# Performance work log

Hardware: AMD Instinct MI355X
Metric: run time of the kernel (lower is better)

Reference implementation:

```python
import jax, jax.numpy as jnp
import numpy as np

B, L, E = 64, 256, 512
H = 1024          # hidden_size
N = 128           # memory_size
HS = 64           # head_size (memory width)
NH = 4            # NTM heads
OUT = 1024        # output_size
TNH = 4           # transformer nhead
IN_DIM = E + NH * HS          # 768
POD = H + NH * HS             # 1280


def ln(x, g, b, eps=1e-5):
    mu = x.mean(-1, keepdims=True)
    v = ((x - mu) ** 2).mean(-1, keepdims=True)
    return (x - mu) / jnp.sqrt(v + eps) * g + b


def setup_inputs() -> dict:
    key = jax.random.key(0)
    ks = iter(jax.random.split(key, 64))
    def w(shape, s=0.05):
        return jax.random.normal(next(ks), shape, jnp.float32) * s
    f32 = jnp.float32
    return dict(
        x_emb=jax.random.normal(next(ks), (B, L, E), f32),
        in_g=jnp.ones(IN_DIM, f32), in_b=jnp.zeros(IN_DIM, f32),
        W_ih=w((4 * H, IN_DIM)), W_hh=w((4 * H, H)),
        b_ih=jnp.zeros(4 * H, f32), b_hh=jnp.zeros(4 * H, f32),
        cn_g=jnp.ones(H, f32), cn_b=jnp.zeros(H, f32),
        W_rk=w((NH * HS, H)), b_rk=jnp.zeros(NH * HS, f32),
        W_wk=w((NH * HS, H)), b_wk=jnp.zeros(NH * HS, f32),
        W_ws=w((NH, H)), b_ws=jnp.zeros(NH, f32),
        W_ev=w((NH * HS, H)), b_ev=jnp.zeros(NH * HS, f32),
        attn_w=w((3 * HS, HS)), attn_b=jnp.zeros(3 * HS, f32),
        attn_ow=w((HS, HS)), attn_ob=jnp.zeros(HS, f32),
        l1_w=w((2 * HS, HS)), l1_b=jnp.zeros(2 * HS, f32),
        l2_w=w((HS, 2 * HS)), l2_b=jnp.zeros(HS, f32),
        tn1_g=jnp.ones(HS, f32), tn1_b=jnp.zeros(HS, f32),
        tn2_g=jnp.ones(HS, f32), tn2_b=jnp.zeros(HS, f32),
        rkn_g=jnp.ones(HS, f32), rkn_b=jnp.zeros(HS, f32),
        wkn_g=jnp.ones(HS, f32), wkn_b=jnp.zeros(HS, f32),
        mn_g=jnp.ones(HS, f32), mn_b=jnp.zeros(HS, f32),
        po_g=jnp.ones(POD, f32), po_b=jnp.zeros(POD, f32),
        W_proj=w((OUT, POD)), b_proj=jnp.zeros(OUT, f32),
    )


def reference(x_emb, in_g, in_b, W_ih, W_hh, b_ih, b_hh, cn_g, cn_b,
              W_rk, b_rk, W_wk, b_wk, W_ws, b_ws, W_ev, b_ev,
              attn_w, attn_b, attn_ow, attn_ob, l1_w, l1_b, l2_w, l2_b,
              tn1_g, tn1_b, tn2_g, tn2_b, rkn_g, rkn_b, wkn_g, wkn_b,
              mn_g, mn_b, po_g, po_b, W_proj, b_proj):
    Bc = x_emb.shape[0]
    dh = HS // TNH

    def tblock(mem):  # [B, N, HS], eval-mode (dropout = identity)
        qkv = mem @ attn_w.T + attn_b
        q, k, v = jnp.split(qkv, 3, axis=-1)
        q = q.reshape(Bc, N, TNH, dh)
        k = k.reshape(Bc, N, TNH, dh)
        v = v.reshape(Bc, N, TNH, dh)
        a = jax.nn.softmax(jnp.einsum('bqhd,bkhd->bhqk', q, k) / jnp.sqrt(jnp.float32(dh)), axis=-1)
        o = jnp.einsum('bhqk,bkhd->bqhd', a, v).reshape(Bc, N, HS)
        o = o @ attn_ow.T + attn_ob
        x = ln(mem + o, tn1_g, tn1_b)
        ff = jax.nn.gelu(x @ l1_w.T + l1_b, approximate=False) @ l2_w.T + l2_b
        return ln(x + ff, tn2_g, tn2_b)

    def step(carry, x_t):
        h, c, mem, rc = carry
        inp = ln(jnp.concatenate([x_t, rc.reshape(Bc, -1)], axis=-1), in_g, in_b)
        gates = inp @ W_ih.T + b_ih + h @ W_hh.T + b_hh  # torch gate order i,f,g,o
        i, f, g, o = jnp.split(gates, 4, axis=-1)
        c = jax.nn.sigmoid(f) * c + jax.nn.sigmoid(i) * jnp.tanh(g)
        h = jax.nn.sigmoid(o) * jnp.tanh(c)
        hn = ln(h, cn_g, cn_b)
        rk = (hn @ W_rk.T + b_rk).reshape(Bc, NH, HS)
        wk = (hn @ W_wk.T + b_wk).reshape(Bc, NH, HS)
        ws = jax.nn.sigmoid(hn @ W_ws.T + b_ws)                    # [B, NH]
        ev = jax.nn.sigmoid(hn @ W_ev.T + b_ev).reshape(Bc, NH, HS)
        # addressing
        mem = tblock(mem)
        mem_n = ln(mem, mn_g, mn_b)
        rk = ln(rk, rkn_g, rkn_b)
        wk = ln(wk, wkn_g, wkn_b)
        rw = jax.nn.softmax(jnp.einsum('bnk,bmk->bnm', rk, mem_n), axis=-1)
        rc = jnp.einsum('bnm,bmh->bnh', rw, mem)
        ww = jax.nn.softmax(jnp.einsum('bnk,bmk->bnm', wk, mem_n), axis=-1)
        erase = jnp.einsum('bnm,bnh->bmh', ww, ev)
        mem = mem * (1.0 - erase)
        add = jnp.einsum('bnm,bnh->bmh', ww, ws[..., None] * wk)
        mem = mem + add
        out = ln(jnp.concatenate([hn, rc.reshape(Bc, -1)], axis=-1), po_g, po_b)
        logits = out @ W_proj.T + b_proj
        return (h, c, mem, rc), logits

    h0 = jnp.zeros((Bc, H), x_emb.dtype)
    c0 = jnp.zeros((Bc, H), x_emb.dtype)
    mem0 = jnp.zeros((Bc, N, HS), x_emb.dtype)
    rc0 = jnp.zeros((Bc, NH, HS), x_emb.dtype)
    (h, c, mem, _), outs = jax.lax.scan(step, (h0, c0, mem0, rc0), jnp.swapaxes(x_emb, 0, 1))
    return jnp.swapaxes(outs, 0, 1), mem, (h[None], c[None])
```

## Files before the change

kernel.cpp:

```cpp
#include <hip/hip_runtime.h>
#include <math.h>

typedef short s8v __attribute__((ext_vector_type(8)));
typedef float f32x4 __attribute__((ext_vector_type(4)));

__device__ inline float sigm(float x) { return 1.0f / (1.0f + expf(-x)); }
__device__ inline float dot4(const float4 a, const float4 b) {
  return a.x*b.x + a.y*b.y + a.z*b.z + a.w*b.w;
}
__device__ inline float wsum(float v) {
#pragma unroll
  for (int o = 32; o > 0; o >>= 1) v += __shfl_xor(v, o, 64);
  return v;
}
__device__ inline short f2bf(float f) {
  unsigned int u = __float_as_uint(f);
  unsigned int r = u + 0x7FFFu + ((u >> 16) & 1u);
  return (short)(r >> 16);
}
__device__ inline float bf2f(short h) {
  return __uint_as_float(((unsigned int)(unsigned short)h) << 16);
}
__device__ inline void storesplit(float v, short* __restrict__ hi,
                                  short* __restrict__ lo, size_t idx) {
  short h = f2bf(v);
  hi[idx] = h;
  lo[idx] = f2bf(v - bf2f(h));
}

template<int LD, int KS>
__device__ __forceinline__ void gemm4(const short* __restrict__ A,
                                      const short* __restrict__ B,
                                      f32x4 acc[4], int lane) {
  int off = (lane & 15) * LD + ((lane >> 4) * 8);
#pragma unroll 4
  for (int kb = 0; kb < KS; kb++) {
    int ko = off + kb*32;
    s8v bb = *(const s8v*)(B + ko);
#pragma unroll
    for (int m = 0; m < 4; m++) {
      s8v aa = *(const s8v*)(A + ko + m*16*LD);
      acc[m] = __builtin_amdgcn_mfma_f32_16x16x32_bf16(aa, bb, acc[m], 0,0,0);
    }
  }
}

__global__ void kprep_g(const float* __restrict__ Wih, const float* __restrict__ Whh,
                        short* __restrict__ WgH, short* __restrict__ WgL) {
  int r = blockIdx.y, k = blockIdx.x*256 + threadIdx.x;
  if (k < 1792) {
    int jt = r >> 6, rr = r & 63, ul = rr >> 2, gi = rr & 3;
    int orow = gi*1024 + jt*16 + ul;
    float v = (k < 768) ? Wih[(size_t)orow*768 + k] : Whh[(size_t)orow*1024 + (k-768)];
    storesplit(v, WgH, WgL, (size_t)r*1792 + k);
  }
}
__global__ void kprep_p(const float* __restrict__ Wp, short* __restrict__ W) {
  int j = blockIdx.y, k = blockIdx.x*256 + threadIdx.x;
  W[(size_t)j*1280 + k] = f2bf(Wp[(size_t)j*1280 + k]);
}
__global__ void kprep_h(const float* __restrict__ Wrk, const float* __restrict__ Wwk,
                        const float* __restrict__ Wev, const float* __restrict__ Wws,
                        short* __restrict__ WhH, short* __restrict__ WhL) {
  int j = blockIdx.y, k = blockIdx.x*256 + threadIdx.x;
  float v;
  if (j < 256)      v = Wrk[(size_t)j*1024 + k];
  else if (j < 512) v = Wwk[(size_t)(j-256)*1024 + k];
  else if (j < 768) v = Wev[(size_t)(j-512)*1024 + k];
  else if (j < 772) v = Wws[(size_t)(j-768)*1024 + k];
  else v = 0.f;
  storesplit(v, WhH, WhL, (size_t)j*1024 + k);
}
__global__ void kprep_q(const float* __restrict__ aw, short* __restrict__ WH,
                        short* __restrict__ WL) {
  int i = blockIdx.x*64 + threadIdx.x;
  storesplit(aw[i], WH, WL, i);
}

__global__ __launch_bounds__(256) void k_prep0(
    const float* __restrict__ x_emb, const float* __restrict__ in_g,
    const float* __restrict__ in_b, short* __restrict__ inbH,
    short* __restrict__ inbL)
{
  __shared__ float rs[4], rq[4];
  int b = blockIdx.x, tid = threadIdx.x, lane = tid & 63, wid = tid >> 6;
  float v3[3]; float s = 0.f, sq = 0.f;
#pragma unroll
  for (int i = 0; i < 3; i++) {
    int k = tid + i * 256;
    float v = (k < 512) ? x_emb[(size_t)b * 256 * 512 + k] : 0.f;
    v3[i] = v; s += v; sq += v * v;
  }
  s = wsum(s); sq = wsum(sq);
  if (lane == 0) { rs[wid] = s; rq[wid] = sq; }
  __syncthreads();
  float ts = rs[0]+rs[1]+rs[2]+rs[3], tq = rq[0]+rq[1]+rq[2]+rq[3];
  float mu = ts / 768.f, var = tq / 768.f - mu * mu;
  float rstd = rsqrtf(var + 1e-5f);
#pragma unroll
  for (int i = 0; i < 3; i++) {
    int k = tid + i * 256;
    storesplit((v3[i] - mu) * rstd * in_g[k] + in_b[k], inbH, inbL, b*1792 + k);
  }
}

__global__ __launch_bounds__(256) void kA(
    const short* __restrict__ inbH, const short* __restrict__ inbL,
    short* __restrict__ inbHn, short* __restrict__ inbLn,
    const short* __restrict__ WgH, const short* __restrict__ WgL,
    const float* __restrict__ b_ih, const float* __restrict__ b_hh,
    float* __restrict__ cbuf, float* __restrict__ hbuf,
    float* __restrict__ hstat, float* __restrict__ gatesP,
    unsigned* __restrict__ tick,
    const short* __restrict__ membH, const short* __restrict__ membL,
    const short* __restrict__ WqH, const short* __restrict__ WqL,
    const float* __restrict__ attn_b,
    const short* __restrict__ pob16, const short* __restrict__ Wp16,
    const float* __restrict__ b_proj,
    float* __restrict__ qkv, float* __restrict__ outs, int t)
{
  __shared__ char poolA[40960];
  __shared__ unsigned sOld;
  int bid = blockIdx.x, tid = threadIdx.x, lane = tid & 63, w = tid >> 6;
  if (bid < 128) {
    if (t >= 256) return;
    short (*sT)[4][2560] = (short(*)[4][2560])poolA;
    int jt = bid & 63, kt = bid >> 6;
    int k0 = kt * 896;
    int srow = tid >> 2, scol = (tid & 3) * 8;
    const short* gAH = inbH + srow*1792 + k0 + scol;
    const short* gAL = inbL + srow*1792 + k0 + scol;
    const short* gBH = WgH + (size_t)(jt*64 + srow)*1792 + k0 + scol;
    const short* gBL = WgL + (size_t)(jt*64 + srow)*1792 + k0 + scol;
    int4 rAH = *(const int4*)gAH, rAL = *(const int4*)gAL;
    int4 rBH = *(const int4*)gBH, rBL = *(const int4*)gBL;
    *(int4*)&sT[0][0][srow*40 + scol] = rAH;
    *(int4*)&sT[0][1][srow*40 + scol] = rAL;
    *(int4*)&sT[0][2][srow*40 + scol] = rBH;
    *(int4*)&sT[0][3][srow*40 + scol] = rBL;
    f32x4 acc[4] = {};
    int arow = lane & 15, akk = (lane >> 4) * 8;
    for (int c = 0; c < 28; ++c) {
      int cur = c & 1;
      if (c < 27) {
        rAH = *(const int4*)(gAH + (c+1)*32);
        rAL = *(const int4*)(gAL + (c+1)*32);
        rBH = *(const int4*)(gBH + (c+1)*32);
        rBL = *(const int4*)(gBL + (c+1)*32);
      }
      __syncthreads();
      s8v bh = *(const s8v*)&sT[cur][2][(w*16 + arow)*40 + akk];
      s8v bl = *(const s8v*)&sT[cur][3][(w*16 + arow)*40 + akk];
#pragma unroll
      for (int ms = 0; ms < 4; ++ms) {
        s8v ah = *(const s8v*)&sT[cur][0][(arow + ms*16)*40 + akk];
        s8v al = *(const s8v*)&sT[cur][1][(arow + ms*16)*40 + akk];
        acc[ms] = __builtin_amdgcn_mfma_f32_16x16x32_bf16(ah, bh, acc[ms], 0,0,0);
        acc[ms] = __builtin_amdgcn_mfma_f32_16x16x32_bf16(al, bh, acc[ms], 0,0,0);
        acc[ms] = __builtin_amdgcn_mfma_f32_16x16x32_bf16(ah, bl, acc[ms], 0,0,0);
      }
      if (c < 27) {
        *(int4*)&sT[cur^1][0][srow*40 + scol] = rAH;
        *(int4*)&sT[cur^1][1][srow*40 + scol] = rAL;
        *(int4*)&sT[cur^1][2][srow*40 + scol] = rBH;
        *(int4*)&sT[cur^1][3][srow*40 + scol] = rBL;
      }
    }
    {
      float* gp = gatesP + (size_t)kt * 262144;
      int j = jt*64 + w*16 + (lane & 15);
#pragma unroll
      for (int ms = 0; ms < 4; ms++)
#pragma unroll
        for (int r = 0; r < 4; r++) {
          int b = ms*16 + (lane>>4)*4 + r;
          gp[b*4096 + j] = acc[ms][r];
        }
    }
    __syncthreads();
    if (tid == 0) {
      __threadfence();
      sOld = __hip_atomic_fetch_add(&tick[jt], 1u, __ATOMIC_ACQ_REL,
                                    __HIP_MEMORY_SCOPE_AGENT);
    }
    __syncthreads();
    if (!(sOld & 1u)) return;
    {
      const float* pp = gatesP + (size_t)(kt^1) * 262144;
      int j = jt*64 + w*16 + (lane & 15);
#pragma unroll
      for (int ms = 0; ms < 4; ms++)
#pragma unroll
        for (int r = 0; r < 4; r++) {
          int b = ms*16 + (lane>>4)*4 + r;
          acc[ms][r] += __hip_atomic_load(&pp[b*4096 + j], __ATOMIC_RELAXED,
                                          __HIP_MEMORY_SCOPE_AGENT);
        }
    }
    float* sC = (float*)poolA;
    float* sRed = (float*)(poolA + 17408);
    __syncthreads();
    {
      int rr = w*16 + (lane & 15);
#pragma unroll
      for (int ms = 0; ms < 4; ms++)
#pragma unroll
        for (int r = 0; r < 4; r++) {
          int b = ms*16 + (lane>>4)*4 + r;
          sC[b*68 + rr] = acc[ms][r];
        }
    }
    __syncthreads();
    {
      int b = tid & 63;
      float sh = 0.f, sh2 = 0.f;
#pragma unroll
      for (int q = 0; q < 4; q++) {
        int ul = (tid >> 6) + q*4;
        int u = jt*16 + ul;
        float gi_ = sC[b*68 + ul*4 + 0] + b_ih[u]        + b_hh[u];
        float gf  = sC[b*68 + ul*4 + 1] + b_ih[1024 + u] + b_hh[1024 + u];
        float gg  = sC[b*68 + ul*4 + 2] + b_ih[2048 + u] + b_hh[2048 + u];
        float go  = sC[b*68 + ul*4 + 3] + b_ih[3072 + u] + b_hh[3072 + u];
        float cn = sigm(gf)*cbuf[b*1024 + u] + sigm(gi_)*tanhf(gg);
        float hh = sigm(go)*tanhf(cn);
        cbuf[b*1024 + u] = cn;
        hbuf[b*1024 + u] = hh;
        storesplit(hh, inbHn, inbLn, b*1792 + 768 + u);
        sh += hh; sh2 += hh*hh;
      }
      sRed[(tid>>6)*64 + b] = sh;
      sRed[256 + (tid>>6)*64 + b] = sh2;
    }
    __syncthreads();
    if (tid < 64) {
      float s0 = sRed[tid]+sRed[64+tid]+sRed[128+tid]+sRed[192+tid];
      float s1 = sRed[256+tid]+sRed[320+tid]+sRed[384+tid]+sRed[448+tid];
      hstat[(tid*64 + jt)*2]     = s0;
      hstat[(tid*64 + jt)*2 + 1] = s1;
    }
  } else if (bid < 192) {
    if (t >= 256) return;
    int b = bid - 128;
    const short* Ah = membH + (size_t)b * 8192;
    const short* Al = membL + (size_t)b * 8192;
    int ao = (w*32 + (lane & 15)) * 64 + (lane >> 4) * 8;
    s8v ah00 = *(const s8v*)(Ah + ao);
    s8v ah01 = *(const s8v*)(Ah + ao + 32);
    s8v ah10 = *(const s8v*)(Ah + ao + 16*64);
    s8v ah11 = *(const s8v*)(Ah + ao + 16*64 + 32);
    s8v al00 = *(const s8v*)(Al + ao);
    s8v al01 = *(const s8v*)(Al + ao + 32);
    s8v al10 = *(const s8v*)(Al + ao + 16*64);
    s8v al11 = *(const s8v*)(Al + ao + 16*64 + 32);
    int bo = (lane & 15) * 64 + (lane >> 4) * 8;
    for (int n = 0; n < 12; n++) {
      s8v bh0 = *(const s8v*)(WqH + bo + n*1024);
      s8v bh1 = *(const s8v*)(WqH + bo + n*1024 + 32);
      s8v bl0 = *(const s8v*)(WqL + bo + n*1024);
      s8v bl1 = *(const s8v*)(WqL + bo + n*1024 + 32);
      f32x4 acc0 = {}, acc1 = {};
      acc0 = __builtin_amdgcn_mfma_f32_16x16x32_bf16(ah00, bh0, acc0, 0,0,0);
      acc0 = __builtin_amdgcn_mfma_f32_16x16x32_bf16(ah01, bh1, acc0, 0,0,0);
      acc0 = __builtin_amdgcn_mfma_f32_16x16x32_bf16(al00, bh0, acc0, 0,0,0);
      acc0 = __builtin_amdgcn_mfma_f32_16x16x32_bf16(al01, bh1, acc0, 0,0,0);
      acc0 = __builtin_amdgcn_mfma_f32_16x16x32_bf16(ah00, bl0, acc0, 0,0,0);
      acc0 = __builtin_amdgcn_mfma_f32_16x16x32_bf16(ah01, bl1, acc0, 0,0,0);
      acc1 = __builtin_amdgcn_mfma_f32_16x16x32_bf16(ah10, bh0, acc1, 0,0,0);
      acc1 = __builtin_amdgcn_mfma_f32_16x16x32_bf16(ah11, bh1, acc1, 0,0,0);
      acc1 = __builtin_amdgcn_mfma_f32_16x16x32_bf16(al10, bh0, acc1, 0,0,0);
      acc1 = __builtin_amdgcn_mfma_f32_16x16x32_bf16(al11, bh1, acc1, 0,0,0);
      acc1 = __builtin_amdgcn_mfma_f32_16x16x32_bf16(ah10, bl0, acc1, 0,0,0);
      acc1 = __builtin_amdgcn_mfma_f32_16x16x32_bf16(ah11, bl1, acc1, 0,0,0);
      int j = n*16 + (lane & 15);
      int ch = j >> 6, jj = j & 63;
      float bv = attn_b[j];
#pragma unroll
      for (int r = 0; r < 4; r++) {
        int m0 = w*32 + (lane>>4)*4 + r;
        qkv[((size_t)(b*3 + ch)*128 + m0)*64 + jj] = acc0[r] + bv;
        qkv[((size_t)(b*3 + ch)*128 + m0 + 16)*64 + jj] = acc1[r] + bv;
      }
    }
  } else {
    if (t == 0) return;
    int jt = bid - 192;
    f32x4 acc[4] = {};
    const short* B = Wp16 + (size_t)(jt*64 + w*16) * 1280;
    gemm4<1280, 40>(pob16, B, acc, lane);
    int j = jt*64 + w*16 + (lane & 15);
    float bv = b_proj[j];
#pragma unroll
    for (int ms = 0; ms < 4; ms++)
#pragma unroll
      for (int r = 0; r < 4; r++) {
        int b = ms*16 + (lane>>4)*4 + r;
        outs[((size_t)b*256 + (t-1))*1024 + j] = acc[ms][r] + bv;
      }
  }
}

__global__ __launch_bounds__(512) void kB(
    float* __restrict__ mem, const float* __restrict__ qkv,
    const float* __restrict__ attn_ow, const float* __restrict__ attn_ob,
    const float* __restrict__ l1w, const float* __restrict__ l1b,
    const float* __restrict__ l2w, const float* __restrict__ l2b,
    const float* __restrict__ tn1g, const float* __restrict__ tn1b,
    const float* __restrict__ tn2g, const float* __restrict__ tn2b,
    const float* __restrict__ hbuf, const float* __restrict__ hstat,
    const float* __restrict__ cn_g, const float* __restrict__ cn_b,
    const short* __restrict__ WhH, const short* __restrict__ WhL,
    float* __restrict__ hp)
{
  __shared__ float pool[35200];
  int bid = blockIdx.x, tid = threadIdx.x;
  int lane = tid & 63, wid = tid >> 6;
  if (bid < 52) {
    int kt = bid & 3, jt = bid >> 2;
    {
      int b2 = tid & 63, part = tid >> 6;
      float s0 = 0.f, s1 = 0.f;
#pragma unroll 4
      for (int m2 = 0; m2 < 8; m2++) {
        int jt2 = part*8 + m2;
        s0 += hstat[(b2*64 + jt2)*2];
        s1 += hstat[(b2*64 + jt2)*2 + 1];
      }
      pool[part*64 + b2] = s0;
      pool[512 + part*64 + b2] = s1;
    }
    __syncthreads();
    if (tid < 64) {
      float ts = 0.f, tq = 0.f;
#pragma unroll
      for (int p2 = 0; p2 < 8; p2++) {
        ts += pool[p2*64 + tid];
        tq += pool[512 + p2*64 + tid];
      }
      float mu = ts / 1024.f;
      pool[1024+tid] = mu;
      pool[1088+tid] = rsqrtf(tq/1024.f - mu*mu + 1e-5f);
    }
    __syncthreads();
    short* sAH = (short*)&pool[1152];
    short* sAL = sAH + 2560;
    int srow = tid >> 3, scol = (tid & 7) * 4;
    int arow = lane & 15, akk = (lane >> 4) * 8;
    f32x4 acc[4] = {};
    for (int c = 0; c < 8; ++c) {
      __syncthreads();
      {
        float mu = pool[1024 + srow], rsd = pool[1088 + srow];
        int kbase = kt*256 + c*32 + scol;
        const float* hpt = hbuf + srow*1024 + kbase;
#pragma unroll
        for (int i = 0; i < 4; i++) {
          float hnv = (hpt[i] - mu) * rsd * cn_g[kbase + i] + cn_b[kbase + i];
          short hh = f2bf(hnv);
          sAH[srow*40 + scol + i] = hh;
          sAL[srow*40 + scol + i] = f2bf(hnv - bf2f(hh));
        }
      }
      __syncthreads();
      if (wid < 4) {
        size_t bo = (size_t)(jt*64 + wid*16 + arow)*1024 + kt*256 + c*32 + akk;
        s8v bh = *(const s8v*)(WhH + bo);
        s8v bl = *(const s8v*)(WhL + bo);
#pragma unroll
        for (int ms = 0; ms < 4; ++ms) {
          s8v ah = *(const s8v*)&sAH[(arow + ms*16)*40 + akk];
          s8v al = *(const s8v*)&sAL[(arow + ms*16)*40 + akk];
          acc[ms] = __builtin_amdgcn_mfma_f32_16x16x32_bf16(ah, bh, acc[ms], 0,0,0);
          acc[ms] = __builtin_amdgcn_mfma_f32_16x16x32_bf16(al, bh, acc[ms], 0,0,0);
          acc[ms] = __builtin_amdgcn_mfma_f32_16x16x32_bf16(ah, bl, acc[ms], 0,0,0);
        }
      }
    }
    if (wid < 4) {
      int j = jt*64 + wid*16 + (lane & 15);
#pragma unroll
      for (int ms = 0; ms < 4; ms++)
#pragma unroll
        for (int r = 0; r < 4; r++) {
          int b2 = ms*16 + (lane>>4)*4 + r;
          hp[(size_t)kt*53248 + b2*832 + j] = acc[ms][r];
        }
    }
    return;
  }
  float* sK  = pool;
  float* sV  = pool + 8704;
  float* sX  = pool + 17408;
  float* sM  = pool + 19584;
  float* sO  = pool + 21760;
  float* sS  = pool + 23936;
  float* sRed= pool + 34176;
  int bb0 = bid - 52;
  int b = bb0 & 63, mt = bb0 >> 6;
  int m0 = mt * 32;
  const float* qb = qkv + (size_t)b*3*8192;
  for (int i = tid*4; i < 8192; i += 2048) {
    *(float4*)&sK[i] = *(const float4*)&qb[8192 + i];
    *(float4*)&sV[i] = *(const float4*)&qb[16384 + i];
  }
  {
    int i = tid*4;
    int m = i >> 6, s = i & 63;
    *(float4*)&sX[m*68+s] = *(const float4*)&qb[m0*64 + i];
    *(float4*)&sM[m*68+s] = *(const float4*)&mem[(size_t)b*8192 + m0*64 + i];
  }
  __syncthreads();
  int m = tid >> 4, hd = (tid >> 2) & 3, q = tid & 3;
  const float* qp = sX + m*68 + hd*16;
  float4 q0 = *(const float4*)(qp),   q1 = *(const float4*)(qp+4);
  float4 q2 = *(const float4*)(qp+8), q3 = *(const float4*)(qp+12);
  int kmb = q * 32;
  float mx = -1e30f;
#pragma unroll 4
  for (int kk = 0; kk < 32; kk++) {
    const float* kp = sK + (kmb+kk)*64 + hd*16;
    float sc = dot4(q0, *(const float4*)kp)     + dot4(q1, *(const float4*)(kp+4))
             + dot4(q2, *(const float4*)(kp+8)) + dot4(q3, *(const float4*)(kp+12));
    mx = fmaxf(mx, sc * 0.25f);
  }
  float4 o0 = {0,0,0,0}, o1 = {0,0,0,0}, o2 = {0,0,0,0}, o3 = {0,0,0,0};
  float sum = 0.f;
#pragma unroll 4
  for (int kk = 0; kk < 32; kk++) {
    const float* kp = sK + (kmb+kk)*64 + hd*16;
    float sc = dot4(q0, *(const float4*)kp)     + dot4(q1, *(const float4*)(kp+4))
             + dot4(q2, *(const float4*)(kp+8)) + dot4(q3, *(const float4*)(kp+12));
    float e = expf(sc * 0.25f - mx);
    sum += e;
    const float* vp = sV + (kmb+kk)*64 + hd*16;
    float4 v0 = *(const float4*)vp,     v1 = *(const float4*)(vp+4);
    float4 v2 = *(const float4*)(vp+8), v3 = *(const float4*)(vp+12);
    o0.x += e*v0.x; o0.y += e*v0.y; o0.z += e*v0.z; o0.w += e*v0.w;
    o1.x += e*v1.x; o1.y += e*v1.y; o1.z += e*v1.z; o1.w += e*v1.w;
    o2.x += e*v2.x; o2.y += e*v2.y; o2.z += e*v2.z; o2.w += e*v2.w;
    o3.x += e*v3.x; o3.y += e*v3.y; o3.z += e*v3.z; o3.w += e*v3.w;
  }
  {
    float* pp = sS + tid*20;
    *(float4*)&pp[0]  = o0; *(float4*)&pp[4]  = o1;
    *(float4*)&pp[8]  = o2; *(float4*)&pp[12] = o3;
    sRed[tid] = mx; sRed[512+tid] = sum;
  }
  __syncthreads();
  if (q == 0) {
    float m1 = sRed[tid+1], m2 = sRed[tid+2], m3 = sRed[tid+3];
    float M = fmaxf(fmaxf(mx, m1), fmaxf(m2, m3));
    float e0 = expf(mx - M), e1 = expf(m1 - M), e2 = expf(m2 - M), e3 = expf(m3 - M);
    float inv = 1.0f / (sum*e0 + sRed[512+tid+1]*e1 + sRed[512+tid+2]*e2
                        + sRed[512+tid+3]*e3);
    const float* p1 = sS + (tid+1)*20;
    const float* p2 = sS + (tid+2)*20;
    const float* p3 = sS + (tid+3)*20;
    float oo[16];
    *(float4*)&oo[0] = o0; *(float4*)&oo[4] = o1;
    *(float4*)&oo[8] = o2; *(float4*)&oo[12] = o3;
    float* op = sO + m*68 + hd*16;
#pragma unroll
    for (int d = 0; d < 16; d++)
      op[d] = (oo[d]*e0 + p1[d]*e1 + p2[d]*e2 + p3[d]*e3) * inv;
  }
  __syncthreads();
  for (int idx = tid; idx < 4096; idx += 512) {
    int j = idx >> 6, s = idx & 63;
    sS[j*68 + s] = attn_ow[idx];
  }
  __syncthreads();
  {
    int mm = tid >> 4, jset = tid & 15;
    float4 orow[16];
#pragma unroll
    for (int r = 0; r < 16; r++) orow[r] = *(const float4*)&sO[mm*68 + r*4];
#pragma unroll
    for (int i = 0; i < 4; i++) {
      int j = jset + 16*i;
      const float* wr = sS + j*68;
      float acc = attn_ob[j];
#pragma unroll
      for (int r = 0; r < 16; r++) acc += dot4(orow[r], *(const float4*)&wr[r*4]);
      sM[mm*68 + j] += acc;
    }
  }
  __syncthreads();
  for (int r = wid; r < 32; r += 8) {
    float v = sM[r*68 + lane];
    float ssum = wsum(v), ssq = wsum(v*v);
    float mu = ssum*(1.f/64), var = ssq*(1.f/64) - mu*mu;
    sX[r*68+lane] = (v - mu)*rsqrtf(var+1e-5f)*tn1g[lane] + tn1b[lane];
  }
  for (int idx = tid; idx < 8192; idx += 512) {
    int f = idx >> 6, s = idx & 63;
    sK[f*68 + s] = l1w[idx];
  }
  for (int idx = tid; idx < 8192; idx += 512) {
    int j = idx >> 7, s = idx & 127;
    sV[j*132 + s] = l2w[idx];
  }
  __syncthreads();
  {
    int mm = tid >> 4, fs = tid & 15;
    float4 xr[16];
#pragma unroll
    for (int r = 0; r < 16; r++) xr[r] = *(const float4*)&sX[mm*68 + r*4];
#pragma unroll 4
    for (int i = 0; i < 8; i++) {
      int f = fs + 16*i;
      const float* wr = sK + f*68;
      float acc = l1b[f];
#pragma unroll
      for (int r = 0; r < 16; r++) acc += dot4(xr[r], *(const float4*)&wr[r*4]);
      sS[mm*132 + f] = 0.5f*acc*(1.0f + erff(acc*0.70710678118654752f));
    }
  }
  __syncthreads();
  {
    int mm = tid >> 4, jset = tid & 15;
    float acc6[4];
#pragma unroll
    for (int i = 0; i < 4; i++) acc6[i] = sX[mm*68 + jset + 16*i] + l2b[jset + 16*i];
#pragma unroll
    for (int h = 0; h < 2; h++) {
      float4 fr[16];
#pragma unroll
      for (int r = 0; r < 16; r++) fr[r] = *(const float4*)&sS[mm*132 + h*64 + r*4];
#pragma unroll
      for (int i = 0; i < 4; i++) {
        int j = jset + 16*i;
        const float* wr = sV + j*132 + h*64;
        float a = 0.f;
#pragma unroll
        for (int r = 0; r < 16; r++) a += dot4(fr[r], *(const float4*)&wr[r*4]);
        acc6[i] += a;
      }
    }
#pragma unroll
    for (int i = 0; i < 4; i++) sO[mm*68 + jset + 16*i] = acc6[i];
  }
  __syncthreads();
  for (int r = wid; r < 32; r += 8) {
    float v = sO[r*68 + lane];
    float ssum = wsum(v), ssq = wsum(v*v);
    float mu = ssum*(1.f/64), var = ssq*(1.f/64) - mu*mu;
    mem[(size_t)b*8192 + (m0+r)*64 + lane] =
        (v - mu)*rsqrtf(var+1e-5f)*tn2g[lane] + tn2b[lane];
  }
}

__global__ __launch_bounds__(512) void kC(
    float* __restrict__ mem, short* __restrict__ membH, short* __restrict__ membL,
    const float* __restrict__ hp, const float* __restrict__ hstat,
    const float* __restrict__ hbuf,
    const float* __restrict__ b_rk, const float* __restrict__ b_wk,
    const float* __restrict__ b_ev, const float* __restrict__ b_ws,
    const float* __restrict__ rkn_g, const float* __restrict__ rkn_b,
    const float* __restrict__ wkn_g, const float* __restrict__ wkn_b,
    const float* __restrict__ cn_g, const float* __restrict__ cn_b,
    const float* __restrict__ mng, const float* __restrict__ mnb,
    const float* __restrict__ pog, const float* __restrict__ pob,
    const float* __restrict__ x_emb, const float* __restrict__ in_g,
    const float* __restrict__ in_b,
    short* __restrict__ inbHn, short* __restrict__ inbLn,
    short* __restrict__ pob16, int tnext)
{
  __shared__ float P[20960];
  float* sMT  = P;
  float* sMN  = P + 8192;
  float* sHn  = P + 16512;
  float* sRk  = P + 17536;
  float* sWk  = P + 17792;
  float* sEv  = P + 18048;
  float* sWs  = P + 18304;
  float* sRw  = P + 18308;
  float* sWw  = P + 18820;
  float* sRc  = P + 19332;
  float* sRcP = P + 19588;
  float* rs   = P + 20100;
  float* rq   = P + 20108;
  float* sHst = P + 20116;
  int b = blockIdx.x, tid = threadIdx.x, lane = tid & 63, wv = tid >> 6;
  for (int i = tid*4; i < 8192; i += 2048)
    *(float4*)&sMT[i] = *(const float4*)&mem[(size_t)b*8192 + i];
  if (wv == 0) {
    float v0 = hstat[(b*64 + lane)*2], v1 = hstat[(b*64 + lane)*2 + 1];
    float s0 = wsum(v0), s1 = wsum(v1);
    if (lane == 0) {
      float mu = s0 / 1024.f;
      sHst[0] = mu;
      sHst[1] = rsqrtf(s1/1024.f - mu*mu + 1e-5f);
    }
  }
  __syncthreads();
  {
    float mu = sHst[0], rstd = sHst[1];
    for (int u = tid; u < 1024; u += 512)
      sHn[u] = (hbuf[b*1024 + u] - mu)*rstd*cn_g[u] + cn_b[u];
  }
  {
    const float* h0 = hp + (size_t)b*832;
    const float* h1 = hp + 53248 + (size_t)b*832;
    const float* h2 = hp + 2*53248 + (size_t)b*832;
    const float* h3 = hp + 3*53248 + (size_t)b*832;
    if (wv < 4) {
      int idx = wv*64 + lane;
      float v = h0[idx] + h1[idx] + h2[idx] + h3[idx] + b_rk[idx];
      float ssum = wsum(v), ssq = wsum(v*v);
      float mu = ssum*(1.f/64), var = ssq*(1.f/64) - mu*mu;
      sRk[idx] = (v - mu)*rsqrtf(var+1e-5f)*rkn_g[lane] + rkn_b[lane];
    } else {
      int idx = (wv-4)*64 + lane;
      float v = h0[256+idx] + h1[256+idx] + h2[256+idx] + h3[256+idx] + b_wk[idx];
      float ssum = wsum(v), ssq = wsum(v*v);
      float mu = ssum*(1.f/64), var = ssq*(1.f/64) - mu*mu;
      sWk[idx] = (v - mu)*rsqrtf(var+1e-5f)*wkn_g[lane] + wkn_b[lane];
    }
    if (tid < 256)
      sEv[tid] = sigm(h0[512+tid] + h1[512+tid] + h2[512+tid] + h3[512+tid] + b_ev[tid]);
    if (tid >= 256 && tid < 260) {
      int n = tid - 256;
      sWs[n] = sigm(h0[768+n] + h1[768+n] + h2[768+n] + h3[768+n] + b_ws[n]);
    }
  }
  for (int r = wv; r < 128; r += 8) {
    float v = sMT[r*64 + lane];
    float ssum = wsum(v), ssq = wsum(v*v);
    float mu = ssum*(1.f/64), var = ssq*(1.f/64) - mu*mu;
    sMN[r*65 + lane] = (v - mu)*rsqrtf(var+1e-5f)*mng[lane] + mnb[lane];
  }
  __syncthreads();
#pragma unroll
  for (int q = 0; q < 2; q++) {
    int idx = tid + q*512;
    int which = idx >> 9;
    int n = (idx >> 7) & 3, m = idx & 127;
    const float* key = (which ? sWk : sRk) + n*64;
    const float* mr = sMN + m*65;
    float acc = 0.f;
#pragma unroll 8
    for (int k = 0; k < 64; k++) acc += key[k]*mr[k];
    (which ? sWw : sRw)[n*128 + m] = acc;
  }
  __syncthreads();
  {
    float* row = (wv < 4) ? (sRw + wv*128) : (sWw + (wv-4)*128);
    float a0 = row[lane], a1 = row[lane+64];
    float mx = fmaxf(a0, a1);
#pragma unroll
    for (int o = 32; o > 0; o >>= 1) mx = fmaxf(mx, __shfl_xor(mx, o, 64));
    float e0 = expf(a0 - mx), e1 = expf(a1 - mx);
    float inv = 1.0f / wsum(e0 + e1);
    row[lane] = e0*inv; row[lane+64] = e1*inv;
  }
  __syncthreads();
  {
    int idx = tid & 255, h2 = tid >> 8;
    int n = idx >> 6, s2 = idx & 63;
    float acc = 0.f;
    for (int mm = h2*64; mm < h2*64 + 64; mm++) acc += sRw[n*128 + mm] * sMT[mm*64 + s2];
    sRcP[tid] = acc;
  }
  __syncthreads();
  if (tid < 256) sRc[tid] = sRcP[tid] + sRcP[256 + tid];
  for (int idx = tid; idx < 8192; idx += 512) {
    int mm = idx >> 6, s2 = idx & 63;
    float er = 0.f, ad = 0.f;
#pragma unroll
    for (int n = 0; n < 4; n++) {
      float w = sWw[n*128 + mm];
      er += w * sEv[n*64 + s2];
      ad += w * sWs[n] * sWk[n*64 + s2];
    }
    float val = sMT[idx]*(1.0f - er) + ad;
    mem[(size_t)b*8192 + idx] = val;
    storesplit(val, membH, membL, (size_t)b*8192 + idx);
  }
  __syncthreads();
  {
    float v5[3]; float s = 0.f, sq = 0.f;
#pragma unroll
    for (int i = 0; i < 3; i++) {
      int k = tid + i*512;
      float v = 0.f;
      if (k < 1280) v = (k < 1024) ? sHn[k] : sRc[k-1024];
      v5[i] = v; s += v; sq += v*v;
    }
    s = wsum(s); sq = wsum(sq);
    if (lane == 0) { rs[wv] = s; rq[wv] = sq; }
    __syncthreads();
    float ts = 0.f, tq = 0.f;
#pragma unroll
    for (int p = 0; p < 8; p++) { ts += rs[p]; tq += rq[p]; }
    float mu = ts/1280.f, var = tq/1280.f - mu*mu;
    float rstd = rsqrtf(var + 1e-5f);
#pragma unroll
    for (int i = 0; i < 3; i++) {
      int k = tid + i*512;
      if (k < 1280) pob16[b*1280 + k] = f2bf((v5[i] - mu)*rstd*pog[k] + pob[k]);
    }
  }
  if (tnext < 256) {
    __syncthreads();
    float v3[2]; float s2 = 0.f, q2 = 0.f;
#pragma unroll
    for (int i = 0; i < 2; i++) {
      int k = tid + i*512;
      float v = 0.f;
      if (k < 768) v = (k < 512) ? x_emb[((size_t)b*256 + tnext)*512 + k] : sRc[k-512];
      v3[i] = v; s2 += v; q2 += v*v;
    }
    s2 = wsum(s2); q2 = wsum(q2);
    if (lane == 0) { rs[wv] = s2; rq[wv] = q2; }
    __syncthreads();
    float ts = 0.f, tq = 0.f;
#pragma unroll
    for (int p = 0; p < 8; p++) { ts += rs[p]; tq += rq[p]; }
    float mu = ts/768.f, var = tq/768.f - mu*mu;
    float rstd = rsqrtf(var + 1e-5f);
#pragma unroll
    for (int i = 0; i < 2; i++) {
      int k = tid + i*512;
      if (k < 768)
        storesplit((v3[i] - mu)*rstd*in_g[k] + in_b[k], inbHn, inbLn, b*1792 + k);
    }
  }
}

__global__ void k_final(const float* __restrict__ mem, const float* __restrict__ hbuf,
                        const float* __restrict__ cbuf, float* __restrict__ out)
{
  int i = blockIdx.x * 256 + threadIdx.x;
  if (i < 524288) out[16777216 + i] = mem[i];
  if (i < 65536) {
    out[17301504 + i] = hbuf[i];
    out[17367040 + i] = cbuf[i];
  }
}

extern "C" void kernel_launch(void* const* d_in, const int* in_sizes, int n_in,
                              void* d_out, int out_size, void* d_ws, size_t ws_size,
                              hipStream_t stream) {
  const float* x_emb  = (const float*)d_in[0];
  const float* in_g   = (const float*)d_in[1];
  const float* in_b   = (const float*)d_in[2];
  const float* W_ih   = (const float*)d_in[3];
  const float* W_hh   = (const float*)d_in[4];
  const float* b_ih   = (const float*)d_in[5];
  const float* b_hh   = (const float*)d_in[6];
  const float* cn_g   = (const float*)d_in[7];
  const float* cn_b   = (const float*)d_in[8];
  const float* W_rk   = (const float*)d_in[9];
  const float* b_rk   = (const float*)d_in[10];
  const float* W_wk   = (const float*)d_in[11];
  const float* b_wk   = (const float*)d_in[12];
  const float* W_ws   = (const float*)d_in[13];
  const float* b_ws   = (const float*)d_in[14];
  const float* W_ev   = (const float*)d_in[15];
  const float* b_ev   = (const float*)d_in[16];
  const float* attn_w = (const float*)d_in[17];
  const float* attn_b = (const float*)d_in[18];
  const float* attn_ow= (const float*)d_in[19];
  const float* attn_ob= (const float*)d_in[20];
  const float* l1_w   = (const float*)d_in[21];
  const float* l1_b   = (const float*)d_in[22];
  const float* l2_w   = (const float*)d_in[23];
  const float* l2_b   = (const float*)d_in[24];
  const float* tn1_g  = (const float*)d_in[25];
  const float* tn1_b  = (const float*)d_in[26];
  const float* tn2_g  = (const float*)d_in[27];
  const float* tn2_b  = (const float*)d_in[28];
  const float* rkn_g  = (const float*)d_in[29];
  const float* rkn_b  = (const float*)d_in[30];
  const float* wkn_g  = (const float*)d_in[31];
  const float* wkn_b  = (const float*)d_in[32];
  const float* mn_g   = (const float*)d_in[33];
  const float* mn_b   = (const float*)d_in[34];
  const float* po_g   = (const float*)d_in[35];
  const float* po_b   = (const float*)d_in[36];
  const float* W_proj = (const float*)d_in[37];
  const float* b_proj = (const float*)d_in[38];

  float* ws = (float*)d_ws;
  float* mem    = ws;
  float* cbuf   = ws + 524288;
  float* hbuf   = ws + 589824;
  float* gatesP = ws + 655360;
  float* hp     = ws + 1179648;
  float* hstat  = ws + 1392640;
  unsigned* tick = (unsigned*)(ws + 1400832);
  float* qkvb   = ws + 1400896;
  short* sb     = (short*)(ws + 2973760);
  short* inbH0 = sb;
  short* inbL0 = sb + 114688;
  short* inbH1 = sb + 229376;
  short* inbL1 = sb + 344064;
  short* membH = sb + 458752;
  short* membL = sb + 983040;
  short* pob16 = sb + 1507328;
  short* WgH   = sb + 1589248;
  short* WgL   = sb + 8929280;
  short* WhH   = sb + 16269312;
  short* WhL   = sb + 17121280;
  short* WqH   = sb + 17973248;
  short* WqL   = sb + 17985536;
  short* Wp16  = sb + 17997824;

  hipMemsetAsync(ws, 0, 655360 * sizeof(float), stream);
  hipMemsetAsync(tick, 0, 256, stream);
  hipMemsetAsync(sb, 0, 1507328 * sizeof(short), stream);

  kprep_g<<<dim3(7, 4096), 256, 0, stream>>>(W_ih, W_hh, WgH, WgL);
  kprep_p<<<dim3(5, 1024), 256, 0, stream>>>(W_proj, Wp16);
  kprep_h<<<dim3(4, 832), 256, 0, stream>>>(W_rk, W_wk, W_ev, W_ws, WhH, WhL);
  kprep_q<<<dim3(192), 64, 0, stream>>>(attn_w, WqH, WqL);
  k_prep0<<<64, 256, 0, stream>>>(x_emb, in_g, in_b, inbH0, inbL0);

  float* outs = (float*)d_out;
  short* bufsH[2] = {inbH0, inbH1};
  short* bufsL[2] = {inbL0, inbL1};
  for (int t = 0; t < 256; t++) {
    kA<<<208, 256, 0, stream>>>(bufsH[t&1], bufsL[t&1], bufsH[(t+1)&1], bufsL[(t+1)&1],
                                WgH, WgL, b_ih, b_hh, cbuf, hbuf, hstat, gatesP, tick,
                                membH, membL, WqH, WqL, attn_b,
                                pob16, Wp16, b_proj, qkvb, outs, t);
    kB<<<308, 512, 0, stream>>>(mem, qkvb, attn_ow, attn_ob,
                                l1_w, l1_b, l2_w, l2_b,
                                tn1_g, tn1_b, tn2_g, tn2_b,
                                hbuf, hstat, cn_g, cn_b, WhH, WhL, hp);
    kC<<<64, 512, 0, stream>>>(mem, membH, membL, hp, hstat, hbuf,
                               b_rk, b_wk, b_ev, b_ws,
                               rkn_g, rkn_b, wkn_g, wkn_b, cn_g, cn_b,
                               mn_g, mn_b, po_g, po_b,
                               x_emb, in_g, in_b,
                               bufsH[(t+1)&1], bufsL[(t+1)&1], pob16, t+1);
  }
  kA<<<208, 256, 0, stream>>>(bufsH[0], bufsL[0], bufsH[1], bufsL[1],
                              WgH, WgL, b_ih, b_hh, cbuf, hbuf, hstat, gatesP, tick,
                              membH, membL, WqH, WqL, attn_b,
                              pob16, Wp16, b_proj, qkvb, outs, 256);
  k_final<<<2048, 256, 0, stream>>>(mem, hbuf, cbuf, (float*)d_out);
}
```

Before: 25.81 ms.

## Move head-projection GEMM into kA behind a device-wide atomic counter wait

The 52 blocks that compute the head projections (hp) from the layer-normed LSTM hidden state move from kB into kA as extra blocks. They spin on a global counter that the 64 LSTM gate blocks increment once they finish writing h and hstat. This lets the projection overlap with the qkv and output-projection work in kA and shrinks kB to the transformer blocks only. It depends on all 260 blocks being co-resident to avoid deadlock, and spin-waiting blocks hold compute units while they wait.

```diff
diff --git a/kernel.cpp b/kernel.cpp
--- a/kernel.cpp
+++ b/kernel.cpp
@@ -111,12 +111,15 @@
     const float* __restrict__ b_ih, const float* __restrict__ b_hh,
     float* __restrict__ cbuf, float* __restrict__ hbuf,
     float* __restrict__ hstat, float* __restrict__ gatesP,
-    unsigned* __restrict__ tick,
+    unsigned* __restrict__ tick, unsigned* __restrict__ gctr,
     const short* __restrict__ membH, const short* __restrict__ membL,
     const short* __restrict__ WqH, const short* __restrict__ WqL,
     const float* __restrict__ attn_b,
     const short* __restrict__ pob16, const short* __restrict__ Wp16,
     const float* __restrict__ b_proj,
+    const float* __restrict__ cn_g, const float* __restrict__ cn_b,
+    const short* __restrict__ WhH, const short* __restrict__ WhL,
+    float* __restrict__ hp,
     float* __restrict__ qkv, float* __restrict__ outs, int t)
 {
   __shared__ char poolA[40960];
@@ -238,6 +241,11 @@
       float s1 = sRed[256+tid]+sRed[320+tid]+sRed[384+tid]+sRed[448+tid];
       hstat[(tid*64 + jt)*2]     = s0;
       hstat[(tid*64 + jt)*2 + 1] = s1;
+    }
+    __syncthreads();
+    if (tid == 0) {
+      __threadfence();
+      __hip_atomic_fetch_add(gctr, 1u, __ATOMIC_RELEASE, __HIP_MEMORY_SCOPE_AGENT);
     }
   } else if (bid < 192) {
     if (t >= 256) return;
@@ -282,7 +290,7 @@
         qkv[((size_t)(b*3 + ch)*128 + m0 + 16)*64 + jj] = acc1[r] + bv;
       }
     }
-  } else {
+  } else if (bid < 208) {
     if (t == 0) return;
     int jt = bid - 192;
     f32x4 acc[4] = {};
@@ -297,6 +305,80 @@
         int b = ms*16 + (lane>>4)*4 + r;
         outs[((size_t)b*256 + (t-1))*1024 + j] = acc[ms][r] + bv;
       }
+  } else {
+    if (t >= 256) return;
+    float* pool = (float*)poolA;
+    if (tid == 0) {
+      unsigned target = 64u * (unsigned)(t + 1);
+      while (__hip_atomic_load(gctr, __ATOMIC_ACQUIRE, __HIP_MEMORY_SCOPE_AGENT) < target)
+        __builtin_amdgcn_s_sleep(2);
+    }
+    __syncthreads();
+    int hb = bid - 208;
+    int kt = hb & 3, jt = hb >> 2;
+    {
+      int b2 = tid & 63, part = tid >> 6;
+      float s0 = 0.f, s1 = 0.f;
+#pragma unroll 4
+      for (int m2 = 0; m2 < 16; m2++) {
+        int jt2 = part*16 + m2;
+        s0 += hstat[(b2*64 + jt2)*2];
+        s1 += hstat[(b2*64 + jt2)*2 + 1];
+      }
+      pool[part*64 + b2] = s0;
+      pool[256 + part*64 + b2] = s1;
+    }
+    __syncthreads();
+    if (tid < 64) {
+      float ts = pool[tid]+pool[64+tid]+pool[128+tid]+pool[192+tid];
+      float tq = pool[256+tid]+pool[320+tid]+pool[384+tid]+pool[448+tid];
+      float mu = ts / 1024.f;
+      pool[512+tid] = mu;
+      pool[576+tid] = rsqrtf(tq/1024.f - mu*mu + 1e-5f);
+    }
+    __syncthreads();
+    short* sAH = (short*)&pool[640];
+    short* sAL = sAH + 2560;
+    int srow = tid >> 2, scol = (tid & 3) * 8;
+    int arow = lane & 15, akk = (lane >> 4) * 8;
+    f32x4 acc[4] = {};
+    for (int c = 0; c < 8; ++c) {
+      __syncthreads();
+      {
+        float mu = pool[512 + srow], rsd = pool[576 + srow];
+        int kbase = kt*256 + c*32 + scol;
+        const float* hpt = hbuf + srow*1024 + kbase;
+#pragma unroll
+        for (int i = 0; i < 8; i++) {
+          float hnv = (hpt[i] - mu) * rsd * cn_g[kbase + i] + cn_b[kbase + i];
+          short hh = f2bf(hnv);
+          sAH[srow*40 + scol + i] = hh;
+          sAL[srow*40 + scol + i] = f2bf(hnv - bf2f(hh));
+        }
+      }
+      __syncthreads();
+      size_t bo = (size_t)(jt*64 + w*16 + arow)*1024 + kt*256 + c*32 + akk;
+      s8v bh = *(const s8v*)(WhH + bo);
+      s8v bl = *(const s8v*)(WhL + bo);
+#pragma unroll
+      for (int ms = 0; ms < 4; ++ms) {
+        s8v ah = *(const s8v*)&sAH[(arow + ms*16)*40 + akk];
+        s8v al = *(const s8v*)&sAL[(arow + ms*16)*40 + akk];
+        acc[ms] = __builtin_amdgcn_mfma_f32_16x16x32_bf16(ah, bh, acc[ms], 0,0,0);
+        acc[ms] = __builtin_amdgcn_mfma_f32_16x16x32_bf16(al, bh, acc[ms], 0,0,0);
+        acc[ms] = __builtin_amdgcn_mfma_f32_16x16x32_bf16(ah, bl, acc[ms], 0,0,0);
+      }
+    }
+    {
+      int j = jt*64 + w*16 + (lane & 15);
+#pragma unroll
+      for (int ms = 0; ms < 4; ms++)
+#pragma unroll
+        for (int r = 0; r < 4; r++) {
+          int b2 = ms*16 + (lane>>4)*4 + r;
+          hp[(size_t)kt*53248 + b2*832 + j] = acc[ms][r];
+        }
+    }
   }
 }
 
@@ -306,88 +388,11 @@
     const float* __restrict__ l1w, const float* __restrict__ l1b,
     const float* __restrict__ l2w, const float* __restrict__ l2b,
     const float* __restrict__ tn1g, const float* __restrict__ tn1b,
-    const float* __restrict__ tn2g, const float* __restrict__ tn2b,
-    const float* __restrict__ hbuf, const float* __restrict__ hstat,
-    const float* __restrict__ cn_g, const float* __restrict__ cn_b,
-    const short* __restrict__ WhH, const short* __restrict__ WhL,
-    float* __restrict__ hp)
+    const float* __restrict__ tn2g, const float* __restrict__ tn2b)
 {
   __shared__ float pool[35200];
   int bid = blockIdx.x, tid = threadIdx.x;
   int lane = tid & 63, wid = tid >> 6;
-  if (bid < 52) {
-    int kt = bid & 3, jt = bid >> 2;
-    {
-      int b2 = tid & 63, part = tid >> 6;
-      float s0 = 0.f, s1 = 0.f;
-#pragma unroll 4
-      for (int m2 = 0; m2 < 8; m2++) {
-        int jt2 = part*8 + m2;
-        s0 += hstat[(b2*64 + jt2)*2];
-        s1 += hstat[(b2*64 + jt2)*2 + 1];
-      }
-      pool[part*64 + b2] = s0;
-      pool[512 + part*64 + b2] = s1;
-    }
-    __syncthreads();
-    if (tid < 64) {
-      float ts = 0.f, tq = 0.f;
-#pragma unroll
-      for (int p2 = 0; p2 < 8; p2++) {
-        ts += pool[p2*64 + tid];
-        tq += pool[512 + p2*64 + tid];
-      }
-      float mu = ts / 1024.f;
-      pool[1024+tid] = mu;
-      pool[1088+tid] = rsqrtf(tq/1024.f - mu*mu + 1e-5f);
-    }
-    __syncthreads();
-    short* sAH = (short*)&pool[1152];
-    short* sAL = sAH + 2560;
-    int srow = tid >> 3, scol = (tid & 7) * 4;
-    int arow = lane & 15, akk = (lane >> 4) * 8;
-    f32x4 acc[4] = {};
-    for (int c = 0; c < 8; ++c) {
-      __syncthreads();
-      {
-        float mu = pool[1024 + srow], rsd = pool[1088 + srow];
-        int kbase = kt*256 + c*32 + scol;
-        const float* hpt = hbuf + srow*1024 + kbase;
-#pragma unroll
-        for (int i = 0; i < 4; i++) {
-          float hnv = (hpt[i] - mu) * rsd * cn_g[kbase + i] + cn_b[kbase + i];
-          short hh = f2bf(hnv);
-          sAH[srow*40 + scol + i] = hh;
-          sAL[srow*40 + scol + i] = f2bf(hnv - bf2f(hh));
-        }
-      }
-      __syncthreads();
-      if (wid < 4) {
-        size_t bo = (size_t)(jt*64 + wid*16 + arow)*1024 + kt*256 + c*32 + akk;
-        s8v bh = *(const s8v*)(WhH + bo);
-        s8v bl = *(const s8v*)(WhL + bo);
-#pragma unroll
-        for (int ms = 0; ms < 4; ++ms) {
-          s8v ah = *(const s8v*)&sAH[(arow + ms*16)*40 + akk];
-          s8v al = *(const s8v*)&sAL[(arow + ms*16)*40 + akk];
-          acc[ms] = __builtin_amdgcn_mfma_f32_16x16x32_bf16(ah, bh, acc[ms], 0,0,0);
-          acc[ms] = __builtin_amdgcn_mfma_f32_16x16x32_bf16(al, bh, acc[ms], 0,0,0);
-          acc[ms] = __builtin_amdgcn_mfma_f32_16x16x32_bf16(ah, bl, acc[ms], 0,0,0);
-        }
-      }
-    }
-    if (wid < 4) {
-      int j = jt*64 + wid*16 + (lane & 15);
-#pragma unroll
-      for (int ms = 0; ms < 4; ms++)
-#pragma unroll
-        for (int r = 0; r < 4; r++) {
-          int b2 = ms*16 + (lane>>4)*4 + r;
-          hp[(size_t)kt*53248 + b2*832 + j] = acc[ms][r];
-        }
-    }
-    return;
-  }
   float* sK  = pool;
   float* sV  = pool + 8704;
   float* sX  = pool + 17408;
@@ -395,8 +400,7 @@
   float* sO  = pool + 21760;
   float* sS  = pool + 23936;
   float* sRed= pool + 34176;
-  int bb0 = bid - 52;
-  int b = bb0 & 63, mt = bb0 >> 6;
+  int b = bid & 63, mt = bid >> 6;
   int m0 = mt * 32;
   const float* qb = qkv + (size_t)b*3*8192;
   for (int i = tid*4; i < 8192; i += 2048) {
@@ -790,8 +794,9 @@
   float* hp     = ws + 1179648;
   float* hstat  = ws + 1392640;
   unsigned* tick = (unsigned*)(ws + 1400832);
-  float* qkvb   = ws + 1400896;
-  short* sb     = (short*)(ws + 2973760);
+  unsigned* gctr = (unsigned*)(ws + 1400896);
+  float* qkvb   = ws + 1400912;
+  short* sb     = (short*)(ws + 2973776);
   short* inbH0 = sb;
   short* inbL0 = sb + 114688;
   short* inbH1 = sb + 229376;
@@ -809,6 +814,7 @@
 
   hipMemsetAsync(ws, 0, 655360 * sizeof(float), stream);
   hipMemsetAsync(tick, 0, 256, stream);
+  hipMemsetAsync(gctr, 0, 64, stream);
   hipMemsetAsync(sb, 0, 1507328 * sizeof(short), stream);
 
   kprep_g<<<dim3(7, 4096), 256, 0, stream>>>(W_ih, W_hh, WgH, WgL);
@@ -821,14 +827,14 @@
   short* bufsH[2] = {inbH0, inbH1};
   short* bufsL[2] = {inbL0, inbL1};
   for (int t = 0; t < 256; t++) {
-    kA<<<208, 256, 0, stream>>>(bufsH[t&1], bufsL[t&1], bufsH[(t+1)&1], bufsL[(t+1)&1],
+    kA<<<260, 256, 0, stream>>>(bufsH[t&1], bufsL[t&1], bufsH[(t+1)&1], bufsL[(t+1)&1],
                                 WgH, WgL, b_ih, b_hh, cbuf, hbuf, hstat, gatesP, tick,
-                                membH, membL, WqH, WqL, attn_b,
-                                pob16, Wp16, b_proj, qkvb, outs, t);
-    kB<<<308, 512, 0, stream>>>(mem, qkvb, attn_ow, attn_ob,
+                                gctr, membH, membL, WqH, WqL, attn_b,
+                                pob16, Wp16, b_proj, cn_g, cn_b, WhH, WhL, hp,
+                                qkvb, outs, t);
+    kB<<<256, 512, 0, stream>>>(mem, qkvb, attn_ow, attn_ob,
                                 l1_w, l1_b, l2_w, l2_b,
-                                tn1_g, tn1_b, tn2_g, tn2_b,
-                                hbuf, hstat, cn_g, cn_b, WhH, WhL, hp);
+                                tn1_g, tn1_b, tn2_g, tn2_b);
     kC<<<64, 512, 0, stream>>>(mem, membH, membL, hp, hstat, hbuf,
                                b_rk, b_wk, b_ev, b_ws,
                                rkn_g, rkn_b, wkn_g, wkn_b, cn_g, cn_b,
@@ -836,9 +842,10 @@
                                x_emb, in_g, in_b,
                                bufsH[(t+1)&1], bufsL[(t+1)&1], pob16, t+1);
   }
-  kA<<<208, 256, 0, stream>>>(bufsH[0], bufsL[0], bufsH[1], bufsL[1],
+  kA<<<260, 256, 0, stream>>>(bufsH[0], bufsL[0], bufsH[1], bufsL[1],
                               WgH, WgL, b_ih, b_hh, cbuf, hbuf, hstat, gatesP, tick,
-                              membH, membL, WqH, WqL, attn_b,
-                              pob16, Wp16, b_proj, qkvb, outs, 256);
+                              gctr, membH, membL, WqH, WqL, attn_b,
+                              pob16, Wp16, b_proj, cn_g, cn_b, WhH, WhL, hp,
+                              qkvb, outs, 256);
   k_final<<<2048, 256, 0, stream>>>(mem, hbuf, cbuf, (float*)d_out);
 }
```

Result: slower. 32.34 ms (+25.3%).
